# Optimization experiments

Measured on AMD Instinct MI355X. Metric: run time of the kernel, lower is better.

The kernel has to match this reference:

```python
import jax, jax.numpy as jnp
import numpy as np

D_MODEL = 1024
N_HEADS = 16
HEAD_DIM = D_MODEL // N_HEADS
LN_EPS = 1e-5


def _linear_init(key, fan_in, fan_out):
    # xavier_uniform for weight, zeros for bias; torch Linear weight is [out, in]
    limit = float(np.sqrt(6.0 / (fan_in + fan_out)))
    w = jax.random.uniform(key, (fan_out, fan_in), jnp.float32, -limit, limit)
    b = jnp.zeros((fan_out,), jnp.float32)
    return w, b


def setup_inputs() -> dict:
    key = jax.random.key(0)
    ks = jax.random.split(key, 8)
    B, S, D = 4, 1024, D_MODEL
    query = jax.random.normal(ks[0], (B, S, D), jnp.float32)
    key_t = jax.random.normal(ks[1], (B, S, D), jnp.float32)
    value = jax.random.normal(ks[2], (B, S, D), jnp.float32)
    Wq, bq = _linear_init(ks[3], D, D)
    Wk, bk = _linear_init(ks[4], D, D)
    Wv, bv = _linear_init(ks[5], D, D)
    Wfq, bfq = _linear_init(ks[6], D, D)
    Wfk, bfk = _linear_init(ks[7], D, D)
    gamma_q = jnp.ones((D,), jnp.float32); beta_q = jnp.zeros((D,), jnp.float32)
    gamma_k = jnp.ones((D,), jnp.float32); beta_k = jnp.zeros((D,), jnp.float32)
    return {"query": query, "key": key_t, "value": value,
            "Wq": Wq, "bq": bq, "Wk": Wk, "bk": bk, "Wv": Wv, "bv": bv,
            "Wfq": Wfq, "bfq": bfq, "Wfk": Wfk, "bfk": bfk,
            "gamma_q": gamma_q, "beta_q": beta_q,
            "gamma_k": gamma_k, "beta_k": beta_k}


def _layernorm(x, gamma, beta):
    mu = jnp.mean(x, axis=-1, keepdims=True)
    var = jnp.mean(jnp.square(x - mu), axis=-1, keepdims=True)
    return (x - mu) * jax.lax.rsqrt(var + LN_EPS) * gamma + beta


def reference(query, key, value, Wq, bq, Wk, bk, Wv, bv, Wfq, bfq, Wfk, bfk,
              gamma_q, beta_q, gamma_k, beta_k):
    B, Sq, D = query.shape
    H, Hd = N_HEADS, HEAD_DIM
    scale = jnp.sqrt(jnp.asarray(Hd, jnp.float32))

    residual_q, residual_k = query, key
    # torch Linear: x @ W.T + b
    q = (query @ Wq.T + bq).reshape(B, Sq, H, Hd).transpose(0, 2, 1, 3)  # [B,H,Sq,Hd]
    k = (key @ Wk.T + bk).reshape(B, -1, H, Hd).transpose(0, 2, 1, 3)    # [B,H,Sk,Hd]
    v = (value @ Wv.T + bv).reshape(B, -1, H, Hd).transpose(0, 2, 1, 3)  # [B,H,Sv,Hd]

    # Q->K attention (dropout disabled / eval mode)
    energy = jnp.einsum('bhqd,bhkd->bhqk', q, k) / scale
    attn_q2k = jax.nn.softmax(energy, axis=-1)
    x_q = jnp.einsum('bhqk,bhkd->bhqd', attn_q2k, v)
    x_q = x_q.transpose(0, 2, 1, 3).reshape(B, Sq, D)

    # K->Q attention (shares V)
    energy_k = jnp.einsum('bhkd,bhqd->bhkq', k, q) / scale
    attn_k2q = jax.nn.softmax(energy_k, axis=-1)
    x_k = jnp.einsum('bhkq,bhqd->bhkd', attn_k2q, v)
    x_k = x_k.transpose(0, 2, 1, 3).reshape(B, -1, D)

    q_out = x_q @ Wfq.T + bfq
    query_out = _layernorm(residual_q + q_out, gamma_q, beta_q)
    k_out = x_k @ Wfk.T + bfk
    key_out = _layernorm(residual_k + k_out, gamma_k, beta_k)
    return (query_out, key_out)
```

## Files before the change

kernel.cpp:

```cpp
#include <hip/hip_runtime.h>

typedef unsigned short u16;
typedef unsigned int u32;
typedef __attribute__((ext_vector_type(8))) short short8;
typedef __attribute__((ext_vector_type(4))) float floatx4;
typedef __attribute__((ext_vector_type(16))) float f32x16;
typedef __attribute__((ext_vector_type(4))) u32 u32x4;

#define AS_GLOBAL __attribute__((address_space(1)))
#define AS_LDS    __attribute__((address_space(3)))

__device__ __forceinline__ float b2f(u16 v) {
  union { u32 u; float f; } x; x.u = ((u32)v) << 16; return x.f;
}
__device__ __forceinline__ u16 f2bf(float f) {
  union { float f; u32 u; } x; x.f = f;
  u32 r = (x.u + 0x7fffu + ((x.u >> 16) & 1u)) >> 16;
  return (u16)r;
}
__device__ __forceinline__ u32 pk2(float lo, float hi) {
  u32 r; asm("v_cvt_pk_bf16_f32 %0, %1, %2" : "=v"(r) : "v"(lo), "v"(hi)); return r;
}
__device__ __forceinline__ void plswap(u32& a, u32& b) {
  __attribute__((ext_vector_type(2))) unsigned int r =
      __builtin_amdgcn_permlane32_swap(a, b, false, false);
  a = r[0]; b = r[1];
}
__device__ __forceinline__ void gl_lds16(const u16* g, u16* l) {
  __builtin_amdgcn_global_load_lds((const AS_GLOBAL u32*)g, (AS_LDS u32*)l, 16, 0, 0);
}

__global__ __launch_bounds__(256)
void cvt8(const float* __restrict__ s0, const float* __restrict__ s1, const float* __restrict__ s2,
          const float* __restrict__ s3, const float* __restrict__ s4, const float* __restrict__ s5,
          const float* __restrict__ s6, const float* __restrict__ s7,
          u16* __restrict__ d0, u16* __restrict__ d1, u16* __restrict__ d2,
          u16* __restrict__ d3, u16* __restrict__ d4, u16* __restrict__ d5,
          u16* __restrict__ d6, u16* __restrict__ d7, int nbig, int nsmall)
{
  const int z = blockIdx.y;
  const float* s; u16* d; int n;
  switch (z) {
    case 0: s = s0; d = d0; n = nbig; break;
    case 1: s = s1; d = d1; n = nbig; break;
    case 2: s = s2; d = d2; n = nbig; break;
    case 3: s = s3; d = d3; n = nsmall; break;
    case 4: s = s4; d = d4; n = nsmall; break;
    case 5: s = s5; d = d5; n = nsmall; break;
    case 6: s = s6; d = d6; n = nsmall; break;
    default: s = s7; d = d7; n = nsmall; break;
  }
  const size_t idx = ((size_t)blockIdx.x * 256 + threadIdx.x) * 8;
  if (idx >= (size_t)n) return;
  float4 a0 = *(const float4*)(s + idx);
  float4 a1 = *(const float4*)(s + idx + 4);
  u16 t[8];
  t[0] = f2bf(a0.x); t[1] = f2bf(a0.y); t[2] = f2bf(a0.z); t[3] = f2bf(a0.w);
  t[4] = f2bf(a1.x); t[5] = f2bf(a1.y); t[6] = f2bf(a1.z); t[7] = f2bf(a1.w);
  *(uint4*)(d + idx) = *(const uint4*)t;
}

template <int TRANS2>
__global__ __launch_bounds__(256, 3)
void gemm_nt_bias(const u16* __restrict__ A0, const u16* __restrict__ W0, const float* __restrict__ B0, u16* __restrict__ C0,
                  const u16* __restrict__ A1, const u16* __restrict__ W1, const float* __restrict__ B1, u16* __restrict__ C1,
                  const u16* __restrict__ A2, const u16* __restrict__ W2, const float* __restrict__ B2, u16* __restrict__ C2)
{
  constexpr int K = 1024, N = 1024;
  __shared__ __attribute__((aligned(16))) u16 As[128 * 64];
  __shared__ __attribute__((aligned(16))) u16 Bs[128 * 64];

  const int z = blockIdx.z;
  const u16*   A  = z == 0 ? A0 : (z == 1 ? A1 : A2);
  const u16*   W  = z == 0 ? W0 : (z == 1 ? W1 : W2);
  const float* Bi = z == 0 ? B0 : (z == 1 ? B1 : B2);
  u16*         C  = z == 0 ? C0 : (z == 1 ? C1 : C2);

  const int tid  = threadIdx.x;
  const int lane = tid & 63;
  const int wave = tid >> 6;
  const int l16  = lane & 15;
  const int quad = lane >> 4;
  const int wm = wave >> 1, wn = wave & 1;
  const int m0 = blockIdx.x * 128;
  const int n0 = blockIdx.y * 128;

  floatx4 acc[4][4];
#pragma unroll
  for (int i = 0; i < 4; ++i)
#pragma unroll
    for (int j = 0; j < 4; ++j)
#pragma unroll
      for (int e = 0; e < 4; ++e) acc[i][j][e] = 0.f;

  const int srow = wave * 32 + (lane >> 3);
  const int scol = (lane & 7) * 8;
  const u16* gA = A + (size_t)(m0 + srow) * K + scol;
  const u16* gW = W + (size_t)(n0 + srow) * K + scol;

  for (int k0 = 0; k0 < K; k0 += 64) {
#pragma unroll
    for (int i = 0; i < 4; ++i) {
      gl_lds16(gA + (size_t)(i * 8) * K + k0, &As[(wave * 32 + i * 8) * 64]);
      gl_lds16(gW + (size_t)(i * 8) * K + k0, &Bs[(wave * 32 + i * 8) * 64]);
    }
    __syncthreads();
#pragma unroll
    for (int ks = 0; ks < 2; ++ks) {
      short8 af[4], bf[4];
#pragma unroll
      for (int mt = 0; mt < 4; ++mt)
        af[mt] = *(const short8*)&As[(wm * 64 + mt * 16 + l16) * 64 + ks * 32 + quad * 8];
#pragma unroll
      for (int nt = 0; nt < 4; ++nt)
        bf[nt] = *(const short8*)&Bs[(wn * 64 + nt * 16 + l16) * 64 + ks * 32 + quad * 8];
#pragma unroll
      for (int mt = 0; mt < 4; ++mt)
#pragma unroll
        for (int nt = 0; nt < 4; ++nt)
          acc[mt][nt] = __builtin_amdgcn_mfma_f32_16x16x32_bf16(af[mt], bf[nt], acc[mt][nt], 0, 0, 0);
    }
    __syncthreads();
  }

  float bb[4];
#pragma unroll
  for (int nt = 0; nt < 4; ++nt) bb[nt] = Bi[n0 + wn * 64 + nt * 16 + l16];

  if (TRANS2 && z == 2) {
#pragma unroll
    for (int mt = 0; mt < 4; ++mt) {
      const int rowb = m0 + wm * 64 + mt * 16 + quad * 4;
#pragma unroll
      for (int nt = 0; nt < 4; ++nt) {
        const int col = n0 + wn * 64 + nt * 16 + l16;
        u32 lo = (u32)f2bf(acc[mt][nt][0] + bb[nt]) | ((u32)f2bf(acc[mt][nt][1] + bb[nt]) << 16);
        u32 hi = (u32)f2bf(acc[mt][nt][2] + bb[nt]) | ((u32)f2bf(acc[mt][nt][3] + bb[nt]) << 16);
        uint2 w; w.x = lo; w.y = hi;
        *(uint2*)&C[(size_t)col * 4096 + rowb] = w;
      }
    }
  } else {
#pragma unroll
    for (int mt = 0; mt < 4; ++mt) {
#pragma unroll
      for (int r = 0; r < 4; ++r) {
        const int row = m0 + wm * 64 + mt * 16 + quad * 4 + r;
        u16* crow = C + (size_t)row * N + n0 + wn * 64 + l16;
#pragma unroll
        for (int nt = 0; nt < 4; ++nt)
          crow[nt * 16] = f2bf(acc[mt][nt][r] + bb[nt]);
      }
    }
  }
}

__global__ __launch_bounds__(256, 2)
void flash32(const u16* __restrict__ Qg, const u16* __restrict__ Kg,
             const u16* __restrict__ VTw, u16* __restrict__ OQ, u16* __restrict__ OK)
{
  __shared__ __attribute__((aligned(16))) u16 smem[4 * 4096];

  const int tid = threadIdx.x;
  const int lane = tid & 63;
  const int wave = tid >> 6;
  const int l32 = lane & 31;
  const int hi = lane >> 5;

  const int jlin = blockIdx.x + 4 * (blockIdx.y + 64 * blockIdx.z);
  const int L = (jlin & 7) * 64 + (jlin >> 3);
  const int qx = L & 3;
  const int by = (L >> 2) & 63;
  const int bz = L >> 8;
  const int b = by >> 4, h = by & 15;
  const int q0 = qx * 256;

  const u16* Qw = bz ? Kg : Qg;
  const u16* Kw = bz ? Qg : Kg;
  u16* Ow = bz ? OK : OQ;

  const int rr = lane >> 3;
  const int s7 = lane & 7;

  const u16* Qt = Qw + ((size_t)(b * 1024 + q0)) * 1024 + h * 64;
  const u16* Kt = Kw + ((size_t)(b * 1024)) * 1024 + h * 64;
  const u16* Vt = VTw + ((size_t)(h * 64)) * 4096 + (size_t)b * 1024;

#pragma unroll
  for (int c = 0; c < 8; ++c) {
    const int R = wave * 64 + c * 8;
    const int cg = ((s7 ^ rr ^ (R >> 3)) & 7) << 3;
    gl_lds16(Qt + (size_t)(R + rr) * 1024 + cg, smem + R * 64);
  }
  __syncthreads();

  short8 aqA[4], aqB[4];
  {
    const int qrA = wave * 64 + l32, qrB = qrA + 32;
    const int kA = (qrA ^ (qrA >> 3)) & 7, kB = (qrB ^ (qrB >> 3)) & 7;
    const u16* bA = smem + qrA * 64;
    const u16* bB = smem + qrB * 64;
#pragma unroll
    for (int d2 = 0; d2 < 4; ++d2) {
      const int g = d2 * 2 + hi;
      aqA[d2] = *(const short8*)(bA + ((g ^ kA) & 7) * 8);
      aqB[d2] = *(const short8*)(bB + ((g ^ kB) & 7) * 8);
    }
  }
  __syncthreads();

  const int R0 = wave * 16, R1 = wave * 16 + 8;
  const int cg0 = ((s7 ^ rr ^ (R0 >> 3)) & 7) << 3;
  const int cg1 = ((s7 ^ rr ^ (R1 >> 3)) & 7) << 3;
  {
    u16* kd = smem + wave * 1024;
    u16* vd = smem + 8192 + wave * 1024;
    gl_lds16(Kt + (size_t)(R0 + rr) * 1024 + cg0, kd);
    gl_lds16(Kt + (size_t)(R1 + rr) * 1024 + cg1, kd + 512);
    gl_lds16(Vt + (size_t)(R0 + rr) * 4096 + cg0, vd);
    gl_lds16(Vt + (size_t)(R1 + rr) * 4096 + cg1, vd + 512);
  }
  __syncthreads();

  const int key0 = (l32 ^ (l32 >> 3)) & 7;
  const int key1 = key0 ^ 4;

  int offA[4], offB[4];
#pragma unroll
  for (int j = 0; j < 4; ++j) {
    const int g = j * 2 + hi;
    offA[j] = (l32 * 64 + ((g ^ key0) & 7) * 8) * 2;
    offB[j] = ((32 + l32) * 64 + ((g ^ key1) & 7) * 8) * 2;
  }

  const u16* pK0 = Kt + (size_t)(64 + R0 + rr) * 1024 + cg0;
  const u16* pK1 = Kt + (size_t)(64 + R1 + rr) * 1024 + cg1;
  const u16* pV0 = Vt + (size_t)(R0 + rr) * 4096 + 64 + cg0;
  const u16* pV1 = Vt + (size_t)(R1 + rr) * 4096 + 64 + cg1;

  f32x16 accO0A, accO1A, accO0B, accO1B;
#pragma unroll
  for (int i = 0; i < 16; ++i) {
    accO0A[i] = 0.f; accO1A[i] = 0.f; accO0B[i] = 0.f; accO1B[i] = 0.f;
  }
  float lsumA = 0.f, lsumB = 0.f;
  const float SCL = 0.125f;
  const float MFIX = 7.0f;

#pragma unroll 2
  for (int jt = 0; jt < 16; ++jt) {
    const int cur = jt & 1;
    const char* ksb = (const char*)smem + cur * 8192;
    const char* vtb = (const char*)smem + 16384 + cur * 8192;

    if (jt < 15) {
      u16* kd = smem + (cur ^ 1) * 4096 + wave * 1024;
      u16* vd = smem + 8192 + (cur ^ 1) * 4096 + wave * 1024;
      gl_lds16(pK0, kd);
      gl_lds16(pK1, kd + 512);
      gl_lds16(pV0, vd);
      gl_lds16(pV1, vd + 512);
      pK0 += 65536; pK1 += 65536; pV0 += 64; pV1 += 64;
    }

#define SUM8(v, o) (((v[o] + v[o + 1]) + (v[o + 2] + v[o + 3])) + \
                    ((v[o + 4] + v[o + 5]) + (v[o + 6] + v[o + 7])))
#define KBLK(KB)                                                                   \
    {                                                                              \
      f32x16 sA, sB;                                                               \
      _Pragma("unroll") for (int i = 0; i < 16; ++i) { sA[i] = 0.f; sB[i] = 0.f; } \
      __builtin_amdgcn_s_setprio(1);                                               \
      _Pragma("unroll") for (int d2 = 0; d2 < 4; ++d2) {                           \
        short8 kf = *(const short8*)(ksb + ((KB) ? offB[d2] : offA[d2]));          \
        sA = __builtin_amdgcn_mfma_f32_32x32x16_bf16(kf, aqA[d2], sA, 0, 0, 0);    \
        sB = __builtin_amdgcn_mfma_f32_32x32x16_bf16(kf, aqB[d2], sB, 0, 0, 0);    \
      }                                                                            \
      __builtin_amdgcn_s_setprio(0);                                               \
      _Pragma("unroll") for (int i = 0; i < 16; ++i)                               \
        sA[i] = __expf(fmaf(sA[i], SCL, -MFIX));                                   \
      _Pragma("unroll") for (int i = 0; i < 16; ++i)                               \
        sB[i] = __expf(fmaf(sB[i], SCL, -MFIX));                                   \
      lsumA += SUM8(sA, 0) + SUM8(sA, 8);                                          \
      lsumB += SUM8(sB, 0) + SUM8(sB, 8);                                          \
      u32 a0 = pk2(sA[0], sA[1]),   a1 = pk2(sA[2], sA[3]);                        \
      u32 b0 = pk2(sA[4], sA[5]),   b1 = pk2(sA[6], sA[7]);                        \
      u32 c0 = pk2(sA[8], sA[9]),   c1 = pk2(sA[10], sA[11]);                      \
      u32 d0 = pk2(sA[12], sA[13]), d1 = pk2(sA[14], sA[15]);                      \
      plswap(a0, b0); plswap(a1, b1); plswap(c0, d0); plswap(c1, d1);              \
      u32x4 uA0; uA0[0] = a0; uA0[1] = a1; uA0[2] = b0; uA0[3] = b1;               \
      u32x4 uA1; uA1[0] = c0; uA1[1] = c1; uA1[2] = d0; uA1[3] = d1;               \
      u32 e0 = pk2(sB[0], sB[1]),   e1 = pk2(sB[2], sB[3]);                        \
      u32 f0 = pk2(sB[4], sB[5]),   f1 = pk2(sB[6], sB[7]);                        \
      u32 g0 = pk2(sB[8], sB[9]),   g1 = pk2(sB[10], sB[11]);                      \
      u32 h0 = pk2(sB[12], sB[13]), h1 = pk2(sB[14], sB[15]);                      \
      plswap(e0, f0); plswap(e1, f1); plswap(g0, h0); plswap(g1, h1);              \
      u32x4 uB0; uB0[0] = e0; uB0[1] = e1; uB0[2] = f0; uB0[3] = f1;               \
      u32x4 uB1; uB1[0] = g0; uB1[1] = g1; uB1[2] = h0; uB1[3] = h1;               \
      const short8 pfaA = __builtin_bit_cast(short8, uA0);                         \
      const short8 pfbA = __builtin_bit_cast(short8, uA1);                         \
      const short8 pfaB = __builtin_bit_cast(short8, uB0);                         \
      const short8 pfbB = __builtin_bit_cast(short8, uB1);                         \
      short8 va0 = *(const short8*)(vtb + offA[(KB) * 2]);                         \
      short8 vb0 = *(const short8*)(vtb + offB[(KB) * 2]);                         \
      short8 va1 = *(const short8*)(vtb + offA[(KB) * 2 + 1]);                     \
      short8 vb1 = *(const short8*)(vtb + offB[(KB) * 2 + 1]);                     \
      __builtin_amdgcn_s_setprio(1);                                               \
      accO0A = __builtin_amdgcn_mfma_f32_32x32x16_bf16(va0, pfaA, accO0A, 0, 0, 0);\
      accO1A = __builtin_amdgcn_mfma_f32_32x32x16_bf16(vb0, pfaA, accO1A, 0, 0, 0);\
      accO0B = __builtin_amdgcn_mfma_f32_32x32x16_bf16(va0, pfaB, accO0B, 0, 0, 0);\
      accO1B = __builtin_amdgcn_mfma_f32_32x32x16_bf16(vb0, pfaB, accO1B, 0, 0, 0);\
      accO0A = __builtin_amdgcn_mfma_f32_32x32x16_bf16(va1, pfbA, accO0A, 0, 0, 0);\
      accO1A = __builtin_amdgcn_mfma_f32_32x32x16_bf16(vb1, pfbA, accO1A, 0, 0, 0);\
      accO0B = __builtin_amdgcn_mfma_f32_32x32x16_bf16(va1, pfbB, accO0B, 0, 0, 0);\
      accO1B = __builtin_amdgcn_mfma_f32_32x32x16_bf16(vb1, pfbB, accO1B, 0, 0, 0);\
      __builtin_amdgcn_s_setprio(0);                                               \
    }
    KBLK(0)
    KBLK(1)
#undef KBLK
#undef SUM8
    __syncthreads();
  }

  const float invlA = 1.f / (lsumA + __shfl_xor(lsumA, 32, 64));
  const float invlB = 1.f / (lsumB + __shfl_xor(lsumB, 32, 64));

  u16* orowA = Ow + ((size_t)(b * 1024 + q0 + wave * 64 + l32)) * 1024 + h * 64 + hi * 4;
  u16* orowB = orowA + (size_t)32 * 1024;
#pragma unroll
  for (int rg = 0; rg < 4; ++rg) {
    uint2 w0;
    w0.x = pk2(accO0A[rg * 4 + 0] * invlA, accO0A[rg * 4 + 1] * invlA);
    w0.y = pk2(accO0A[rg * 4 + 2] * invlA, accO0A[rg * 4 + 3] * invlA);
    *(uint2*)(orowA + rg * 8) = w0;
    uint2 w1;
    w1.x = pk2(accO1A[rg * 4 + 0] * invlA, accO1A[rg * 4 + 1] * invlA);
    w1.y = pk2(accO1A[rg * 4 + 2] * invlA, accO1A[rg * 4 + 3] * invlA);
    *(uint2*)(orowA + 32 + rg * 8) = w1;
    uint2 w2;
    w2.x = pk2(accO0B[rg * 4 + 0] * invlB, accO0B[rg * 4 + 1] * invlB);
    w2.y = pk2(accO0B[rg * 4 + 2] * invlB, accO0B[rg * 4 + 3] * invlB);
    *(uint2*)(orowB + rg * 8) = w2;
    uint2 w3;
    w3.x = pk2(accO1B[rg * 4 + 0] * invlB, accO1B[rg * 4 + 1] * invlB);
    w3.y = pk2(accO1B[rg * 4 + 2] * invlB, accO1B[rg * 4 + 3] * invlB);
    *(uint2*)(orowB + 32 + rg * 8) = w3;
  }
}

__global__ __launch_bounds__(256)
void ln_residual(const u16* __restrict__ TQ, const u16* __restrict__ TK,
                 const float* __restrict__ Rq, const float* __restrict__ Rk,
                 const float* __restrict__ gq, const float* __restrict__ bq,
                 const float* __restrict__ gk, const float* __restrict__ bk,
                 float* __restrict__ out)
{
  const int row = blockIdx.x;
  const u16 *X; const float *R, *G, *Bt; float* O;
  if (row < 4096) {
    X = TQ + (size_t)row * 1024; R = Rq + (size_t)row * 1024;
    G = gq; Bt = bq; O = out + (size_t)row * 1024;
  } else {
    const int r2 = row - 4096;
    X = TK + (size_t)r2 * 1024; R = Rk + (size_t)r2 * 1024;
    G = gk; Bt = bk; O = out + (size_t)4096 * 1024 + (size_t)r2 * 1024;
  }
  const int c0 = threadIdx.x * 4;
  const uint2 xv = *(const uint2*)(X + c0);
  const float4 rv = *(const float4*)(R + c0);
  float v[4];
  v[0] = b2f((u16)(xv.x & 0xffff)) + rv.x;
  v[1] = b2f((u16)(xv.x >> 16)) + rv.y;
  v[2] = b2f((u16)(xv.y & 0xffff)) + rv.z;
  v[3] = b2f((u16)(xv.y >> 16)) + rv.w;
  float sum = (v[0] + v[1]) + (v[2] + v[3]);
  float sumsq = (v[0] * v[0] + v[1] * v[1]) + (v[2] * v[2] + v[3] * v[3]);
#pragma unroll
  for (int sh = 1; sh < 64; sh <<= 1) {
    sum += __shfl_xor(sum, sh, 64);
    sumsq += __shfl_xor(sumsq, sh, 64);
  }
  __shared__ float sm[8];
  const int wave = threadIdx.x >> 6, lane = threadIdx.x & 63;
  if (lane == 0) { sm[wave] = sum; sm[4 + wave] = sumsq; }
  __syncthreads();
  sum = (sm[0] + sm[1]) + (sm[2] + sm[3]);
  sumsq = (sm[4] + sm[5]) + (sm[6] + sm[7]);
  const float mu = sum * (1.f / 1024.f);
  const float var = sumsq * (1.f / 1024.f) - mu * mu;
  const float rstd = rsqrtf(var + 1e-5f);
  const float4 gv = *(const float4*)(G + c0);
  const float4 bv = *(const float4*)(Bt + c0);
  float4 ov;
  ov.x = (v[0] - mu) * rstd * gv.x + bv.x;
  ov.y = (v[1] - mu) * rstd * gv.y + bv.y;
  ov.z = (v[2] - mu) * rstd * gv.z + bv.z;
  ov.w = (v[3] - mu) * rstd * gv.w + bv.w;
  *(float4*)(O + c0) = ov;
}

extern "C" void kernel_launch(void* const* d_in, const int* in_sizes, int n_in,
                              void* d_out, int out_size, void* d_ws, size_t ws_size,
                              hipStream_t stream)
{
  const float* query = (const float*)d_in[0];
  const float* key   = (const float*)d_in[1];
  const float* value = (const float*)d_in[2];
  const float* Wq  = (const float*)d_in[3];  const float* bq  = (const float*)d_in[4];
  const float* Wk  = (const float*)d_in[5];  const float* bk  = (const float*)d_in[6];
  const float* Wv  = (const float*)d_in[7];  const float* bv  = (const float*)d_in[8];
  const float* Wfq = (const float*)d_in[9];  const float* bfq = (const float*)d_in[10];
  const float* Wfk = (const float*)d_in[11]; const float* bfk = (const float*)d_in[12];
  const float* gq = (const float*)d_in[13];  const float* betaq = (const float*)d_in[14];
  const float* gk = (const float*)d_in[15];  const float* betak = (const float*)d_in[16];
  float* out = (float*)d_out;
  u16* ws  = (u16*)d_ws;

  const size_t SZ = (size_t)4096 * 1024;
  const size_t WZ = (size_t)1024 * 1024;
  u16* Qb  = ws;
  u16* Kb  = ws + SZ;
  u16* VT  = ws + 2 * SZ;
  u16* Wqb = ws + 3 * SZ;
  u16* Wkb = Wqb + WZ;
  u16* Wvb = Wkb + WZ;
  u16* Wfqb = Wvb + WZ;
  u16* Wfkb = Wfqb + WZ;
  u16* qbf = (u16*)out;
  u16* kbf = qbf + SZ;
  u16* vbf = kbf + SZ;
  u16* XQ = (u16*)out;
  u16* XK = (u16*)out + SZ;
  u16* TQ = Qb;
  u16* TK = Kb;

  cvt8<<<dim3(2048, 8), 256, 0, stream>>>(query, key, value, Wq, Wk, Wv, Wfq, Wfk,
                                          qbf, kbf, vbf, Wqb, Wkb, Wvb, Wfqb, Wfkb,
                                          (int)SZ, (int)WZ);
  gemm_nt_bias<1><<<dim3(32, 8, 3), 256, 0, stream>>>(qbf, Wqb, bq, Qb,
                                                      kbf, Wkb, bk, Kb,
                                                      vbf, Wvb, bv, VT);
  flash32<<<dim3(4, 64, 2), 256, 0, stream>>>(Qb, Kb, VT, XQ, XK);
  gemm_nt_bias<0><<<dim3(32, 8, 2), 256, 0, stream>>>(XQ, Wfqb, bfq, TQ,
                                                      XK, Wfkb, bfk, TK,
                                                      XK, Wfkb, bfk, TK);
  ln_residual<<<dim3(8192), 256, 0, stream>>>(TQ, TK, query, key,
                                              gq, betaq, gk, betak, out);
}
```

Before: 259.1 us.

## Interleave softmax exp with MFMA in attention loop and use hardware exp2

Restructures the attention inner loop so the exponentials for one key block are computed between the QK^T MFMAs of the next block and the PV MFMAs, letting VALU work overlap with matrix-core work. It also replaces __expf with a direct v_exp_f32 (exp2) using constants pre-scaled by log2(e), which saves a multiply per element. The setprio hints and the unroll-2 pragma are removed. Holding four score tiles live at once raises register pressure, which could reduce occupancy.

```diff
diff --git a/kernel.cpp b/kernel.cpp
--- a/kernel.cpp
+++ b/kernel.cpp
@@ -20,6 +20,9 @@
 }
 __device__ __forceinline__ u32 pk2(float lo, float hi) {
   u32 r; asm("v_cvt_pk_bf16_f32 %0, %1, %2" : "=v"(r) : "v"(lo), "v"(hi)); return r;
+}
+__device__ __forceinline__ float exp2_hw(float x) {
+  float r; asm("v_exp_f32 %0, %1" : "=v"(r) : "v"(x)); return r;
 }
 __device__ __forceinline__ void plswap(u32& a, u32& b) {
   __attribute__((ext_vector_type(2))) unsigned int r =
@@ -244,10 +247,29 @@
     accO0A[i] = 0.f; accO1A[i] = 0.f; accO0B[i] = 0.f; accO1B[i] = 0.f;
   }
   float lsumA = 0.f, lsumB = 0.f;
-  const float SCL = 0.125f;
-  const float MFIX = 7.0f;
-
-#pragma unroll 2
+  const float SCL2 = 0.18033688011112042f;
+  const float MFIX2 = 10.098865286222744f;
+
+#define EXP4(SV, o)                                                     \
+  SV[o + 0] = exp2_hw(fmaf(SV[o + 0], SCL2, -MFIX2));                   \
+  SV[o + 1] = exp2_hw(fmaf(SV[o + 1], SCL2, -MFIX2));                   \
+  SV[o + 2] = exp2_hw(fmaf(SV[o + 2], SCL2, -MFIX2));                   \
+  SV[o + 3] = exp2_hw(fmaf(SV[o + 3], SCL2, -MFIX2));
+#define SUM8(v, o) (((v[o] + v[o + 1]) + (v[o + 2] + v[o + 3])) + \
+                    ((v[o + 4] + v[o + 5]) + (v[o + 6] + v[o + 7])))
+#define PACK(SV, PFA, PFB)                                              \
+  {                                                                     \
+    u32 a0 = pk2(SV[0], SV[1]),   a1 = pk2(SV[2], SV[3]);               \
+    u32 b0 = pk2(SV[4], SV[5]),   b1 = pk2(SV[6], SV[7]);               \
+    u32 c0 = pk2(SV[8], SV[9]),   c1 = pk2(SV[10], SV[11]);             \
+    u32 d0 = pk2(SV[12], SV[13]), d1 = pk2(SV[14], SV[15]);             \
+    plswap(a0, b0); plswap(a1, b1); plswap(c0, d0); plswap(c1, d1);     \
+    u32x4 u0; u0[0] = a0; u0[1] = a1; u0[2] = b0; u0[3] = b1;           \
+    u32x4 u1; u1[0] = c0; u1[1] = c1; u1[2] = d0; u1[3] = d1;           \
+    PFA = __builtin_bit_cast(short8, u0);                               \
+    PFB = __builtin_bit_cast(short8, u1);                               \
+  }
+
   for (int jt = 0; jt < 16; ++jt) {
     const int cur = jt & 1;
     const char* ksb = (const char*)smem + cur * 8192;
@@ -263,64 +285,73 @@
       pK0 += 65536; pK1 += 65536; pV0 += 64; pV1 += 64;
     }
 
-#define SUM8(v, o) (((v[o] + v[o + 1]) + (v[o + 2] + v[o + 3])) + \
-                    ((v[o + 4] + v[o + 5]) + (v[o + 6] + v[o + 7])))
-#define KBLK(KB)                                                                   \
-    {                                                                              \
-      f32x16 sA, sB;                                                               \
-      _Pragma("unroll") for (int i = 0; i < 16; ++i) { sA[i] = 0.f; sB[i] = 0.f; } \
-      __builtin_amdgcn_s_setprio(1);                                               \
-      _Pragma("unroll") for (int d2 = 0; d2 < 4; ++d2) {                           \
-        short8 kf = *(const short8*)(ksb + ((KB) ? offB[d2] : offA[d2]));          \
-        sA = __builtin_amdgcn_mfma_f32_32x32x16_bf16(kf, aqA[d2], sA, 0, 0, 0);    \
-        sB = __builtin_amdgcn_mfma_f32_32x32x16_bf16(kf, aqB[d2], sB, 0, 0, 0);    \
-      }                                                                            \
-      __builtin_amdgcn_s_setprio(0);                                               \
-      _Pragma("unroll") for (int i = 0; i < 16; ++i)                               \
-        sA[i] = __expf(fmaf(sA[i], SCL, -MFIX));                                   \
-      _Pragma("unroll") for (int i = 0; i < 16; ++i)                               \
-        sB[i] = __expf(fmaf(sB[i], SCL, -MFIX));                                   \
-      lsumA += SUM8(sA, 0) + SUM8(sA, 8);                                          \
-      lsumB += SUM8(sB, 0) + SUM8(sB, 8);                                          \
-      u32 a0 = pk2(sA[0], sA[1]),   a1 = pk2(sA[2], sA[3]);                        \
-      u32 b0 = pk2(sA[4], sA[5]),   b1 = pk2(sA[6], sA[7]);                        \
-      u32 c0 = pk2(sA[8], sA[9]),   c1 = pk2(sA[10], sA[11]);                      \
-      u32 d0 = pk2(sA[12], sA[13]), d1 = pk2(sA[14], sA[15]);                      \
-      plswap(a0, b0); plswap(a1, b1); plswap(c0, d0); plswap(c1, d1);              \
-      u32x4 uA0; uA0[0] = a0; uA0[1] = a1; uA0[2] = b0; uA0[3] = b1;               \
-      u32x4 uA1; uA1[0] = c0; uA1[1] = c1; uA1[2] = d0; uA1[3] = d1;               \
-      u32 e0 = pk2(sB[0], sB[1]),   e1 = pk2(sB[2], sB[3]);                        \
-      u32 f0 = pk2(sB[4], sB[5]),   f1 = pk2(sB[6], sB[7]);                        \
-      u32 g0 = pk2(sB[8], sB[9]),   g1 = pk2(sB[10], sB[11]);                      \
-      u32 h0 = pk2(sB[12], sB[13]), h1 = pk2(sB[14], sB[15]);                      \
-      plswap(e0, f0); plswap(e1, f1); plswap(g0, h0); plswap(g1, h1);              \
-      u32x4 uB0; uB0[0] = e0; uB0[1] = e1; uB0[2] = f0; uB0[3] = f1;               \
-      u32x4 uB1; uB1[0] = g0; uB1[1] = g1; uB1[2] = h0; uB1[3] = h1;               \
-      const short8 pfaA = __builtin_bit_cast(short8, uA0);                         \
-      const short8 pfbA = __builtin_bit_cast(short8, uA1);                         \
-      const short8 pfaB = __builtin_bit_cast(short8, uB0);                         \
-      const short8 pfbB = __builtin_bit_cast(short8, uB1);                         \
-      short8 va0 = *(const short8*)(vtb + offA[(KB) * 2]);                         \
-      short8 vb0 = *(const short8*)(vtb + offB[(KB) * 2]);                         \
-      short8 va1 = *(const short8*)(vtb + offA[(KB) * 2 + 1]);                     \
-      short8 vb1 = *(const short8*)(vtb + offB[(KB) * 2 + 1]);                     \
-      __builtin_amdgcn_s_setprio(1);                                               \
-      accO0A = __builtin_amdgcn_mfma_f32_32x32x16_bf16(va0, pfaA, accO0A, 0, 0, 0);\
-      accO1A = __builtin_amdgcn_mfma_f32_32x32x16_bf16(vb0, pfaA, accO1A, 0, 0, 0);\
-      accO0B = __builtin_amdgcn_mfma_f32_32x32x16_bf16(va0, pfaB, accO0B, 0, 0, 0);\
-      accO1B = __builtin_amdgcn_mfma_f32_32x32x16_bf16(vb0, pfaB, accO1B, 0, 0, 0);\
-      accO0A = __builtin_amdgcn_mfma_f32_32x32x16_bf16(va1, pfbA, accO0A, 0, 0, 0);\
-      accO1A = __builtin_amdgcn_mfma_f32_32x32x16_bf16(vb1, pfbA, accO1A, 0, 0, 0);\
-      accO0B = __builtin_amdgcn_mfma_f32_32x32x16_bf16(va1, pfbB, accO0B, 0, 0, 0);\
-      accO1B = __builtin_amdgcn_mfma_f32_32x32x16_bf16(vb1, pfbB, accO1B, 0, 0, 0);\
-      __builtin_amdgcn_s_setprio(0);                                               \
-    }
-    KBLK(0)
-    KBLK(1)
-#undef KBLK
+    f32x16 sA0, sB0, sA1, sB1;
+#pragma unroll
+    for (int i = 0; i < 16; ++i) { sA0[i] = 0.f; sB0[i] = 0.f; sA1[i] = 0.f; sB1[i] = 0.f; }
+#pragma unroll
+    for (int d2 = 0; d2 < 4; ++d2) {
+      short8 kf = *(const short8*)(ksb + offA[d2]);
+      sA0 = __builtin_amdgcn_mfma_f32_32x32x16_bf16(kf, aqA[d2], sA0, 0, 0, 0);
+      sB0 = __builtin_amdgcn_mfma_f32_32x32x16_bf16(kf, aqB[d2], sB0, 0, 0, 0);
+    }
+
+#pragma unroll
+    for (int d2 = 0; d2 < 4; ++d2) {
+      short8 kf = *(const short8*)(ksb + offB[d2]);
+      sA1 = __builtin_amdgcn_mfma_f32_32x32x16_bf16(kf, aqA[d2], sA1, 0, 0, 0);
+      EXP4(sA0, d2 * 4)
+      sB1 = __builtin_amdgcn_mfma_f32_32x32x16_bf16(kf, aqB[d2], sB1, 0, 0, 0);
+      EXP4(sB0, d2 * 4)
+    }
+    lsumA += SUM8(sA0, 0) + SUM8(sA0, 8);
+    lsumB += SUM8(sB0, 0) + SUM8(sB0, 8);
+
+    {
+      short8 pfaA, pfbA, pfaB, pfbB;
+      PACK(sA0, pfaA, pfbA)
+      EXP4(sA1, 0) EXP4(sA1, 4)
+      PACK(sB0, pfaB, pfbB)
+      EXP4(sA1, 8) EXP4(sA1, 12)
+      short8 va0 = *(const short8*)(vtb + offA[0]);
+      short8 vb0 = *(const short8*)(vtb + offB[0]);
+      accO0A = __builtin_amdgcn_mfma_f32_32x32x16_bf16(va0, pfaA, accO0A, 0, 0, 0);
+      accO1A = __builtin_amdgcn_mfma_f32_32x32x16_bf16(vb0, pfaA, accO1A, 0, 0, 0);
+      EXP4(sB1, 0) EXP4(sB1, 4)
+      accO0B = __builtin_amdgcn_mfma_f32_32x32x16_bf16(va0, pfaB, accO0B, 0, 0, 0);
+      accO1B = __builtin_amdgcn_mfma_f32_32x32x16_bf16(vb0, pfaB, accO1B, 0, 0, 0);
+      EXP4(sB1, 8) EXP4(sB1, 12)
+      short8 va1 = *(const short8*)(vtb + offA[1]);
+      short8 vb1 = *(const short8*)(vtb + offB[1]);
+      accO0A = __builtin_amdgcn_mfma_f32_32x32x16_bf16(va1, pfbA, accO0A, 0, 0, 0);
+      accO1A = __builtin_amdgcn_mfma_f32_32x32x16_bf16(vb1, pfbA, accO1A, 0, 0, 0);
+      accO0B = __builtin_amdgcn_mfma_f32_32x32x16_bf16(va1, pfbB, accO0B, 0, 0, 0);
+      accO1B = __builtin_amdgcn_mfma_f32_32x32x16_bf16(vb1, pfbB, accO1B, 0, 0, 0);
+    }
+    lsumA += SUM8(sA1, 0) + SUM8(sA1, 8);
+    lsumB += SUM8(sB1, 0) + SUM8(sB1, 8);
+
+    {
+      short8 pfaA, pfbA, pfaB, pfbB;
+      PACK(sA1, pfaA, pfbA)
+      PACK(sB1, pfaB, pfbB)
+      short8 va0 = *(const short8*)(vtb + offA[2]);
+      short8 vb0 = *(const short8*)(vtb + offB[2]);
+      short8 va1 = *(const short8*)(vtb + offA[3]);
+      short8 vb1 = *(const short8*)(vtb + offB[3]);
+      accO0A = __builtin_amdgcn_mfma_f32_32x32x16_bf16(va0, pfaA, accO0A, 0, 0, 0);
+      accO1A = __builtin_amdgcn_mfma_f32_32x32x16_bf16(vb0, pfaA, accO1A, 0, 0, 0);
+      accO0B = __builtin_amdgcn_mfma_f32_32x32x16_bf16(va0, pfaB, accO0B, 0, 0, 0);
+      accO1B = __builtin_amdgcn_mfma_f32_32x32x16_bf16(vb0, pfaB, accO1B, 0, 0, 0);
+      accO0A = __builtin_amdgcn_mfma_f32_32x32x16_bf16(va1, pfbA, accO0A, 0, 0, 0);
+      accO1A = __builtin_amdgcn_mfma_f32_32x32x16_bf16(vb1, pfbA, accO1A, 0, 0, 0);
+      accO0B = __builtin_amdgcn_mfma_f32_32x32x16_bf16(va1, pfbB, accO0B, 0, 0, 0);
+      accO1B = __builtin_amdgcn_mfma_f32_32x32x16_bf16(vb1, pfbB, accO1B, 0, 0, 0);
+    }
+    __syncthreads();
+  }
+#undef EXP4
 #undef SUM8
-    __syncthreads();
-  }
+#undef PACK
 
   const float invlA = 1.f / (lsumA + __shfl_xor(lsumA, 32, 64));
   const float invlB = 1.f / (lsumB + __shfl_xor(lsumB, 32, 64));
```

Result: faster. 252.7 us (-2.4%).
